# Kernel optimization log

Measured on AMD Instinct MI355X. Metric: run time of the kernel, lower is better.

The kernel has to match this reference:

```python
import jax, jax.numpy as jnp
import numpy as np

B, DIM, HEADS, AGENT = 16, 256, 8, 49
POOL = 7  # int(sqrt(agent_num))


def _pool_matrix(size, out):
    # PyTorch AdaptiveAvgPool2d bin boundaries: start=floor(i*size/out), end=ceil((i+1)*size/out)
    P = np.zeros((out, size), np.float32)
    for i in range(out):
        s = (i * size) // out
        e = -((-(i + 1) * size) // out)
        P[i, s:e] = 1.0 / (e - s)
    return jnp.asarray(P)


def _forward(x, Wq, Wkv, Wproj, bproj, Wdwc, bdwc,
             an_bias, na_bias, ah_bias, aw_bias, ha_bias, wa_bias, H, W):
    b, c, h, w = x.shape
    n = H * W
    head_dim = c // HEADS
    scale = head_dim ** -0.5
    xt = x.reshape(b, c, n).transpose(0, 2, 1)            # [b, n, c]
    q = xt @ Wq.T                                          # [b, n, c]
    kv = xt @ Wkv.T
    k, v = jnp.split(kv, 2, axis=-1)
    # agent tokens: adaptive avg pool of q over the HxW grid -> 7x7
    qimg = q.reshape(b, H, W, c)
    Ph, Pw = _pool_matrix(H, POOL), _pool_matrix(W, POOL)
    agent = jnp.einsum('ph,qw,bhwc->bpqc', Ph, Pw, qimg).reshape(b, AGENT, c)

    def to_heads(t):
        return t.reshape(b, -1, HEADS, head_dim).transpose(0, 2, 1, 3)

    qh, kh, vh, ah = to_heads(q), to_heads(k), to_heads(v), to_heads(agent)

    # stage 1: agent -> kv attention with interpolated position bias
    pb1 = jax.image.resize(an_bias, (HEADS, AGENT, H, W), method='bilinear').reshape(HEADS, AGENT, n)
    pb2 = (ah_bias + aw_bias).reshape(1, HEADS, AGENT, n)
    pos_bias = pb1[None] + pb2                             # [1/b, h, 49, n]
    agent_attn = jax.nn.softmax(jnp.einsum('bhad,bhnd->bhan', ah * scale, kh) + pos_bias, axis=-1)
    agent_v = jnp.einsum('bhan,bhnd->bhad', agent_attn, vh)  # [b, h, 49, d]

    # stage 2: query -> agent attention
    ab1 = jax.image.resize(na_bias, (HEADS, AGENT, H, W), method='bilinear').reshape(HEADS, AGENT, n).transpose(0, 2, 1)
    ab2 = (ha_bias + wa_bias).reshape(1, HEADS, n, AGENT)
    agent_bias = ab1[None] + ab2                           # [1/b, h, n, 49]
    q_attn = jax.nn.softmax(jnp.einsum('bhnd,bhad->bhna', qh * scale, ah) + agent_bias, axis=-1)
    out = jnp.einsum('bhna,bhad->bhnd', q_attn, agent_v).transpose(0, 2, 1, 3).reshape(b, n, c)

    # depthwise conv residual on v
    vimg = vh.transpose(0, 2, 1, 3).reshape(b, H, W, c).transpose(0, 3, 1, 2)  # [b, c, H, W]
    dw = jax.lax.conv_general_dilated(vimg, Wdwc, (1, 1), 'SAME',
                                      feature_group_count=c,
                                      dimension_numbers=('NCHW', 'OIHW', 'NCHW'))
    dw = dw + bdwc[None, :, None, None]
    out = out + dw.transpose(0, 2, 3, 1).reshape(b, n, c)
    out = out @ Wproj.T + bproj
    return out.transpose(0, 2, 1).reshape(b, c, h, w)


def setup_inputs() -> dict:
    key = jax.random.key(0)
    ks = jax.random.split(key, 12)
    s = 0.02
    return {
        'x': jax.random.normal(ks[0], (B, DIM, 64, 64), jnp.float32),
        'Wq': jax.random.normal(ks[1], (DIM, DIM), jnp.float32) * s,
        'Wkv': jax.random.normal(ks[2], (2 * DIM, DIM), jnp.float32) * s,
        'Wproj': jax.random.normal(ks[3], (DIM, DIM), jnp.float32) * s,
        'bproj': jnp.zeros((DIM,), jnp.float32),
        'Wdwc': jax.random.normal(ks[4], (DIM, 1, 3, 3), jnp.float32) * s,
        'bdwc': jnp.zeros((DIM,), jnp.float32),
        'an_bias': jax.random.normal(ks[5], (HEADS, AGENT, 7, 7), jnp.float32) * s,
        'na_bias': jax.random.normal(ks[6], (HEADS, AGENT, 7, 7), jnp.float32) * s,
        'ah_bias': jax.random.normal(ks[7], (1, HEADS, AGENT, 64, 1), jnp.float32) * s,
        'aw_bias': jax.random.normal(ks[8], (1, HEADS, AGENT, 1, 64), jnp.float32) * s,
        'ha_bias': jax.random.normal(ks[9], (1, HEADS, 64, 1, AGENT), jnp.float32) * s,
        'wa_bias': jax.random.normal(ks[10], (1, HEADS, 1, 64, AGENT), jnp.float32) * s,
        'H': 64,
        'W': 64,
    }


def reference(x, Wq, Wkv, Wproj, bproj, Wdwc, bdwc,
              an_bias, na_bias, ah_bias, aw_bias, ha_bias, wa_bias, H, W):
    return _forward(x, Wq, Wkv, Wproj, bproj, Wdwc, bdwc,
                    an_bias, na_bias, ah_bias, aw_bias, ha_bias, wa_bias, H, W)
```

## Files before the change

### kernel.cpp

```cpp
#include <hip/hip_runtime.h>
#include <hip/hip_bf16.h>
#include <stdint.h>

using bf16 = __hip_bfloat16;

#define SCALE 0.17677669529663687f

typedef short short8 __attribute__((ext_vector_type(8)));
typedef float f32x4 __attribute__((ext_vector_type(4)));

__device__ __forceinline__ float bf2f(bf16 v) { return __bfloat162float(v); }

__device__ __forceinline__ unsigned short f2bf(float f) {
    unsigned int u = __float_as_uint(f);
    unsigned int r = u + 0x7fffu + ((u >> 16) & 1u);
    return (unsigned short)(r >> 16);
}

__device__ __forceinline__ void load8bf(const bf16* p, float* f) {
    uint4 u = *reinterpret_cast<const uint4*>(p);
    f[0] = __uint_as_float(u.x << 16); f[1] = __uint_as_float(u.x & 0xffff0000u);
    f[2] = __uint_as_float(u.y << 16); f[3] = __uint_as_float(u.y & 0xffff0000u);
    f[4] = __uint_as_float(u.z << 16); f[5] = __uint_as_float(u.z & 0xffff0000u);
    f[6] = __uint_as_float(u.w << 16); f[7] = __uint_as_float(u.w & 0xffff0000u);
}

__device__ __forceinline__ void gload16(const void* g, void* l) {
    __builtin_amdgcn_global_load_lds(
        (const __attribute__((address_space(1))) void*)g,
        (__attribute__((address_space(3))) void*)l, 16, 0, 0);
}

__global__ __launch_bounds__(256) void convert_w(
    const float* __restrict__ Wq, const float* __restrict__ Wkv,
    const float* __restrict__ Wp,
    bf16* __restrict__ Wqkv_bf, bf16* __restrict__ Wp_bf)
{
    int row = blockIdx.x, tid = threadIdx.x;
    const float* src; bf16* dst;
    if (row < 768) {
        src = (row < 256) ? Wq + (size_t)row * 256 : Wkv + (size_t)(row - 256) * 256;
        dst = Wqkv_bf + (size_t)row * 256;
    } else {
        src = Wp + (size_t)(row - 768) * 256;
        dst = Wp_bf + (size_t)(row - 768) * 256;
    }
    *reinterpret_cast<unsigned short*>(dst + tid) = f2bf(src[tid]);
}

__global__ __launch_bounds__(256) void x_to_bf16T(
    const float* __restrict__ x, bf16* __restrict__ xT)
{
    __shared__ float t[64][65];
    const int b = blockIdx.z, pos0 = blockIdx.x * 64, c0 = blockIdx.y * 64;
    const int tid = threadIdx.x;
    const int cc = tid >> 6, p = tid & 63;
    #pragma unroll
    for (int i = 0; i < 16; ++i)
        t[cc + 4 * i][p] = x[((size_t)(b * 256 + c0 + cc + 4 * i)) * 4096 + pos0 + p];
    __syncthreads();
    const int pl = tid >> 2, qd = tid & 3;
    unsigned short tmp[16];
    #pragma unroll
    for (int j = 0; j < 16; ++j) tmp[j] = f2bf(t[qd * 16 + j][pl]);
    uint4* dst = reinterpret_cast<uint4*>(xT + ((size_t)(b * 4096 + pos0 + pl)) * 256 + c0 + qd * 16);
    dst[0] = reinterpret_cast<const uint4*>(tmp)[0];
    dst[1] = reinterpret_cast<const uint4*>(tmp)[1];
}

__global__ __launch_bounds__(256) void qkv_mfma(
    const bf16* __restrict__ xT, const bf16* __restrict__ Wqkv,
    bf16* __restrict__ q, bf16* __restrict__ k, bf16* __restrict__ v)
{
    __shared__ __align__(16) short As[128 * 32];
    __shared__ __align__(16) short Bs[128 * 32];
    const int b = blockIdx.x >> 5;
    const int m0 = (blockIdx.x & 31) * 128;
    const int j0 = blockIdx.y * 128;
    const int tid = threadIdx.x;
    const int w = tid >> 6, lane = tid & 63;
    const int wm = w & 1, wn = w >> 1;
    const int quad = lane >> 4, ln = lane & 15;

    const short* Ag = (const short*)xT + ((size_t)(b * 4096 + m0)) * 256;
    const short* Bg = (const short*)Wqkv + (size_t)j0 * 256;
    const int ldrow = lane >> 2;
    const int ldcol = (lane & 3) * 8;

    f32x4 acc[4][4] = {};

    for (int k0 = 0; k0 < 256; k0 += 32) {
        __syncthreads();
        #pragma unroll
        for (int p = 0; p < 2; ++p) {
            int row = w * 32 + p * 16;
            gload16(Ag + (size_t)(row + ldrow) * 256 + k0 + ldcol, As + row * 32);
            gload16(Bg + (size_t)(row + ldrow) * 256 + k0 + ldcol, Bs + row * 32);
        }
        __syncthreads();
        short8 af[4], bfr[4];
        #pragma unroll
        for (int mi = 0; mi < 4; ++mi)
            af[mi] = *reinterpret_cast<const short8*>(&As[(wm * 64 + mi * 16 + ln) * 32 + quad * 8]);
        #pragma unroll
        for (int ni = 0; ni < 4; ++ni)
            bfr[ni] = *reinterpret_cast<const short8*>(&Bs[(wn * 64 + ni * 16 + ln) * 32 + quad * 8]);
        #pragma unroll
        for (int mi = 0; mi < 4; ++mi)
            #pragma unroll
            for (int ni = 0; ni < 4; ++ni)
                acc[mi][ni] = __builtin_amdgcn_mfma_f32_16x16x32_bf16(
                    af[mi], bfr[ni], acc[mi][ni], 0, 0, 0);
    }

    bf16* dst; int cb;
    if (j0 < 256)      { dst = q; cb = j0; }
    else if (j0 < 512) { dst = k; cb = j0 - 256; }
    else               { dst = v; cb = j0 - 512; }
    #pragma unroll
    for (int mi = 0; mi < 4; ++mi)
        #pragma unroll
        for (int r = 0; r < 4; ++r) {
            int pos = m0 + wm * 64 + mi * 16 + quad * 4 + r;
            unsigned short* o = reinterpret_cast<unsigned short*>(
                dst + ((size_t)(b * 4096 + pos)) * 256 + cb + wn * 64 + ln);
            #pragma unroll
            for (int ni = 0; ni < 4; ++ni)
                o[ni * 16] = f2bf(acc[mi][ni][r]);
        }
}

__global__ __launch_bounds__(256) void pool_agent(
    const bf16* __restrict__ q, float* __restrict__ agent)
{
    int bid = blockIdx.x;
    int b = bid / 49, a = bid % 49;
    int py = a / 7, px = a % 7;
    int ys = (py * 64) / 7, ye = ((py + 1) * 64 + 6) / 7;
    int xs = (px * 64) / 7, xe = ((px + 1) * 64 + 6) / 7;
    int ch = threadIdx.x;
    float s = 0.f;
    for (int y = ys; y < ye; ++y)
        for (int x = xs; x < xe; ++x)
            s += bf2f(q[((size_t)(b * 4096) + y * 64 + x) * 256 + ch]);
    agent[((size_t)(b * 49) + a) * 256 + ch] = s / (float)((ye - ys) * (xe - xs));
}

__global__ __launch_bounds__(256) void make_pbias(
    const float* __restrict__ an, const float* __restrict__ ahb,
    const float* __restrict__ awb, float* __restrict__ pbias)
{
    int bid = blockIdx.x;
    __shared__ float bb[49], ay[64], ax[64];
    int tid = threadIdx.x;
    if (tid < 49) bb[tid] = an[(size_t)bid * 49 + tid];
    if (tid < 64) {
        ay[tid] = ahb[(size_t)bid * 64 + tid];
        ax[tid] = awb[(size_t)bid * 64 + tid];
    }
    __syncthreads();
    for (int it = 0; it < 16; ++it) {
        int pos = it * 256 + tid;
        int y = pos >> 6, x = pos & 63;
        float fy = (y + 0.5f) * (7.f / 64.f) - 0.5f; fy = fminf(fmaxf(fy, 0.f), 6.f);
        float fx = (x + 0.5f) * (7.f / 64.f) - 0.5f; fx = fminf(fmaxf(fx, 0.f), 6.f);
        int y0 = (int)fy, x0 = (int)fx;
        int y1 = min(y0 + 1, 6), x1 = min(x0 + 1, 6);
        float wy = fy - y0, wx = fx - x0;
        float val = (1.f - wy) * ((1.f - wx) * bb[y0 * 7 + x0] + wx * bb[y0 * 7 + x1])
                  + wy * ((1.f - wx) * bb[y1 * 7 + x0] + wx * bb[y1 * 7 + x1]);
        pbias[(size_t)bid * 4096 + pos] = val + ay[y] + ax[x];
    }
}

__global__ __launch_bounds__(256) void make_abias(
    const float* __restrict__ na, const float* __restrict__ hab,
    const float* __restrict__ wab, float* __restrict__ abiasT)
{
    int bid = blockIdx.x;
    int h = bid / 49, a = bid % 49;
    __shared__ float bb[49], hy[64], wx_[64];
    int tid = threadIdx.x;
    if (tid < 49) bb[tid] = na[(size_t)bid * 49 + tid];
    if (tid < 64) {
        hy[tid]  = hab[((size_t)(h * 64) + tid) * 49 + a];
        wx_[tid] = wab[((size_t)(h * 64) + tid) * 49 + a];
    }
    __syncthreads();
    for (int it = 0; it < 16; ++it) {
        int pos = it * 256 + tid;
        int y = pos >> 6, x = pos & 63;
        float fy = (y + 0.5f) * (7.f / 64.f) - 0.5f; fy = fminf(fmaxf(fy, 0.f), 6.f);
        float fx = (x + 0.5f) * (7.f / 64.f) - 0.5f; fx = fminf(fmaxf(fx, 0.f), 6.f);
        int y0 = (int)fy, x0 = (int)fx;
        int y1 = min(y0 + 1, 6), x1 = min(x0 + 1, 6);
        float wy = fy - y0, wxv = fx - x0;
        float val = (1.f - wy) * ((1.f - wxv) * bb[y0 * 7 + x0] + wxv * bb[y0 * 7 + x1])
                  + wy * ((1.f - wxv) * bb[y1 * 7 + x0] + wxv * bb[y1 * 7 + x1]);
        abiasT[(size_t)bid * 4096 + pos] = val + hy[y] + wx_[x];
    }
}

__global__ __launch_bounds__(256) void stage1(
    const float* __restrict__ agent, const bf16* __restrict__ k,
    const bf16* __restrict__ v, const float* __restrict__ pbias,
    float* __restrict__ part_O, float* __restrict__ part_sum)
{
    const int bid = blockIdx.x;
    const int split = bid & 7, h = (bid >> 3) & 7, b = bid >> 6;
    const int tid = threadIdx.x;
    __shared__ float e_lds[64 * 129];

    const int n_loc = tid & 127;
    const int half  = __builtin_amdgcn_readfirstlane(tid >> 7);
    const int a0 = half * 25, na = half ? 24 : 25;
    const int wv   = __builtin_amdgcn_readfirstlane(tid >> 6);
    const int lane = tid & 63;
    const int aL = lane < 49 ? lane : 48;

    float o[8] = {0.f, 0.f, 0.f, 0.f, 0.f, 0.f, 0.f, 0.f};
    float sacc = 0.f;

    for (int tile = 0; tile < 4; ++tile) {
        const int nbase = split * 512 + tile * 128;
        __syncthreads();
        {
            const int n_glob = nbase + n_loc;
            float kf[32];
            const bf16* kr = k + ((size_t)(b * 4096) + n_glob) * 256 + h * 32;
            load8bf(kr, kf); load8bf(kr + 8, kf + 8);
            load8bf(kr + 16, kf + 16); load8bf(kr + 24, kf + 24);
            const float* aqb = agent + ((size_t)(b * 49) + a0) * 256 + h * 32;
            const float* pbb = pbias + ((size_t)(h * 49) + a0) * 4096 + n_glob;
            for (int ai = 0; ai < na; ++ai) {
                const float* aq = aqb + (size_t)ai * 256;
                float dot = 0.f;
                #pragma unroll
                for (int d = 0; d < 32; ++d) dot = fmaf(aq[d], kf[d], dot);
                float s = dot * SCALE + pbb[(size_t)ai * 4096];
                e_lds[(a0 + ai) * 129 + n_loc] = __expf(s);
            }
        }
        __syncthreads();
        {
            const uint4* vrow = reinterpret_cast<const uint4*>(
                v + ((size_t)(b * 4096) + nbase) * 256 + h * 32 + wv * 8);
            for (int nn = 0; nn < 128; ++nn) {
                float e = e_lds[aL * 129 + nn];
                uint4 pk = vrow[(size_t)nn * 32];
                float vf[8];
                vf[0] = __uint_as_float(pk.x << 16); vf[1] = __uint_as_float(pk.x & 0xffff0000u);
                vf[2] = __uint_as_float(pk.y << 16); vf[3] = __uint_as_float(pk.y & 0xffff0000u);
                vf[4] = __uint_as_float(pk.z << 16); vf[5] = __uint_as_float(pk.z & 0xffff0000u);
                vf[6] = __uint_as_float(pk.w << 16); vf[7] = __uint_as_float(pk.w & 0xffff0000u);
                #pragma unroll
                for (int j = 0; j < 8; ++j) o[j] = fmaf(e, vf[j], o[j]);
                sacc += e;
            }
        }
    }
    if (lane < 49) {
        float* dst = part_O + ((size_t)((b * 8 + h) * 8 + split)) * 1568 + lane * 32 + wv * 8;
        float4 w0 = make_float4(o[0], o[1], o[2], o[3]);
        float4 w1 = make_float4(o[4], o[5], o[6], o[7]);
        *reinterpret_cast<float4*>(dst)     = w0;
        *reinterpret_cast<float4*>(dst + 4) = w1;
        if (wv == 0)
            part_sum[((b * 8 + h) * 8 + split) * 49 + lane] = sacc;
    }
}

__global__ __launch_bounds__(256) void stage1_fin(
    const float* __restrict__ part_O, const float* __restrict__ part_sum,
    float* __restrict__ agent_v)
{
    int bh = blockIdx.x;
    __shared__ float inv[49];
    int tid = threadIdx.x;
    if (tid < 49) {
        float s = 0.f;
        #pragma unroll
        for (int sp = 0; sp < 8; ++sp) s += part_sum[(bh * 8 + sp) * 49 + tid];
        inv[tid] = 1.f / s;
    }
    __syncthreads();
    for (int idx = tid; idx < 1568; idx += 256) {
        float o = 0.f;
        #pragma unroll
        for (int sp = 0; sp < 8; ++sp) o += part_O[((size_t)(bh * 8) + sp) * 1568 + idx];
        agent_v[(size_t)bh * 1568 + idx] = o * inv[idx >> 5];
    }
}

__global__ __launch_bounds__(256) void stage2(
    const bf16* __restrict__ q, const bf16* __restrict__ v,
    const float* __restrict__ agent, const float* __restrict__ agent_v,
    const float* __restrict__ abiasT, const float* __restrict__ wdwc,
    const float* __restrict__ bdwc, bf16* __restrict__ mid)
{
    const int bh = blockIdx.x;
    const int b = bh >> 3, h = bh & 7;
    const int pos = blockIdx.y * 256 + threadIdx.x;

    const float* agb = agent + ((size_t)(b * 49)) * 256 + h * 32;
    const float* avb = agent_v + (size_t)bh * 1568;
    const float* abb = abiasT + (size_t)(h * 49) * 4096 + pos;
    const float* wdb = wdwc + (size_t)(h * 32) * 9;
    const float* bdb = bdwc + h * 32;

    float qv[32];
    {
        const bf16* qr = q + ((size_t)(b * 4096) + pos) * 256 + h * 32;
        #pragma unroll
        for (int u = 0; u < 4; ++u) {
            float f[8]; load8bf(qr + u * 8, f);
            #pragma unroll
            for (int d = 0; d < 8; ++d) qv[u * 8 + d] = f[d] * SCALE;
        }
    }

    float sum = 0.f;
    float acc[32];
    #pragma unroll
    for (int d = 0; d < 32; ++d) acc[d] = 0.f;

    for (int a = 0; a < 49; ++a) {
        const float* ag = agb + (size_t)a * 256;
        const float* av = avb + a * 32;
        float t = abb[(size_t)a * 4096];
        #pragma unroll
        for (int d = 0; d < 32; ++d) t = fmaf(qv[d], ag[d], t);
        float e = __expf(t);
        sum += e;
        #pragma unroll
        for (int d = 0; d < 32; ++d) acc[d] = fmaf(e, av[d], acc[d]);
    }
    float inv = 1.f / sum;
    #pragma unroll
    for (int d = 0; d < 32; ++d) acc[d] *= inv;

    int y = pos >> 6, x = pos & 63;
    #pragma unroll
    for (int dy = -1; dy <= 1; ++dy) {
        int yy = y + dy; if (yy < 0 || yy > 63) continue;
        #pragma unroll
        for (int dx = -1; dx <= 1; ++dx) {
            int xx = x + dx; if (xx < 0 || xx > 63) continue;
            const bf16* vr = v + ((size_t)(b * 4096) + yy * 64 + xx) * 256 + h * 32;
            int widx = (dy + 1) * 3 + (dx + 1);
            #pragma unroll
            for (int u = 0; u < 4; ++u) {
                float f[8]; load8bf(vr + u * 8, f);
                #pragma unroll
                for (int d = 0; d < 8; ++d)
                    acc[u * 8 + d] = fmaf(wdb[(u * 8 + d) * 9 + widx], f[d], acc[u * 8 + d]);
            }
        }
    }
    #pragma unroll
    for (int d = 0; d < 32; ++d) acc[d] += bdb[d];

    bf16* dst = mid + ((size_t)(b * 4096) + pos) * 256 + h * 32;
    #pragma unroll
    for (int u = 0; u < 4; ++u) {
        ushort4 w;
        w.x = f2bf(acc[u * 8 + 0]);
        w.y = f2bf(acc[u * 8 + 1]);
        w.z = f2bf(acc[u * 8 + 2]);
        w.w = f2bf(acc[u * 8 + 3]);
        ushort4 w2;
        w2.x = f2bf(acc[u * 8 + 4]);
        w2.y = f2bf(acc[u * 8 + 5]);
        w2.z = f2bf(acc[u * 8 + 6]);
        w2.w = f2bf(acc[u * 8 + 7]);
        *reinterpret_cast<ushort4*>(dst + u * 8)     = w;
        *reinterpret_cast<ushort4*>(dst + u * 8 + 4) = w2;
    }
}

__global__ __launch_bounds__(256) void proj_mfma(
    const bf16* __restrict__ mid, const bf16* __restrict__ Wp,
    const float* __restrict__ bp, float* __restrict__ out)
{
    __shared__ __align__(16) short As[128 * 32];
    __shared__ __align__(16) short Bs[128 * 32];
    const int m0 = blockIdx.x * 128;
    const int b  = blockIdx.y >> 5;
    const int n0 = (blockIdx.y & 31) * 128;
    const int tid = threadIdx.x;
    const int w = tid >> 6, lane = tid & 63;
    const int wm = w & 1, wn = w >> 1;
    const int quad = lane >> 4, ln = lane & 15;

    const short* Ag = (const short*)Wp + (size_t)m0 * 256;
    const short* Bg = (const short*)mid + ((size_t)(b * 4096 + n0)) * 256;
    const int ldrow = lane >> 2;
    const int ldcol = (lane & 3) * 8;

    f32x4 acc[4][4] = {};

    for (int k0 = 0; k0 < 256; k0 += 32) {
        __syncthreads();
        #pragma unroll
        for (int p = 0; p < 2; ++p) {
            int row = w * 32 + p * 16;
            gload16(Ag + (size_t)(row + ldrow) * 256 + k0 + ldcol, As + row * 32);
            gload16(Bg + (size_t)(row + ldrow) * 256 + k0 + ldcol, Bs + row * 32);
        }
        __syncthreads();
        short8 af[4], bfr[4];
        #pragma unroll
        for (int mi = 0; mi < 4; ++mi)
            af[mi] = *reinterpret_cast<const short8*>(&As[(wm * 64 + mi * 16 + ln) * 32 + quad * 8]);
        #pragma unroll
        for (int ni = 0; ni < 4; ++ni)
            bfr[ni] = *reinterpret_cast<const short8*>(&Bs[(wn * 64 + ni * 16 + ln) * 32 + quad * 8]);
        #pragma unroll
        for (int mi = 0; mi < 4; ++mi)
            #pragma unroll
            for (int ni = 0; ni < 4; ++ni)
                acc[mi][ni] = __builtin_amdgcn_mfma_f32_16x16x32_bf16(
                    af[mi], bfr[ni], acc[mi][ni], 0, 0, 0);
    }

    #pragma unroll
    for (int mi = 0; mi < 4; ++mi)
        #pragma unroll
        for (int r = 0; r < 4; ++r) {
            int ch = m0 + wm * 64 + mi * 16 + quad * 4 + r;
            float bias = bp[ch];
            float* o = out + ((size_t)(b * 256 + ch)) * 4096 + n0 + wn * 64 + ln;
            #pragma unroll
            for (int ni = 0; ni < 4; ++ni)
                o[ni * 16] = acc[mi][ni][r] + bias;
        }
}

extern "C" void kernel_launch(void* const* d_in, const int* in_sizes, int n_in,
                              void* d_out, int out_size, void* d_ws, size_t ws_size,
                              hipStream_t stream)
{
    const float* x       = (const float*)d_in[0];
    const float* Wq      = (const float*)d_in[1];
    const float* Wkv     = (const float*)d_in[2];
    const float* Wproj   = (const float*)d_in[3];
    const float* bproj   = (const float*)d_in[4];
    const float* Wdwc    = (const float*)d_in[5];
    const float* bdwc    = (const float*)d_in[6];
    const float* an_bias = (const float*)d_in[7];
    const float* na_bias = (const float*)d_in[8];
    const float* ah_bias = (const float*)d_in[9];
    const float* aw_bias = (const float*)d_in[10];
    const float* ha_bias = (const float*)d_in[11];
    const float* wa_bias = (const float*)d_in[12];

    char* ws = (char*)d_ws;
    bf16*  q      = (bf16*)(ws + 0);
    bf16*  k      = (bf16*)(ws + 33554432);
    bf16*  v      = (bf16*)(ws + 67108864);
    bf16*  xT     = (bf16*)(ws + 100663296);
    float* part_O   = (float*)(ws + 100663296);
    float* part_sum = (float*)(ws + 100663296 + 6422528);
    bf16*  mid    = (bf16*)(ws + 100663296);
    float* agent  = (float*)(ws + 134217728);
    float* agentv = (float*)(ws + 135020544);
    float* pbias  = (float*)(ws + 135823360);
    float* abiasT = (float*)(ws + 142245888);
    bf16*  Wqkv_bf = (bf16*)(ws + 148668416);
    bf16*  Wp_bf   = (bf16*)(ws + 149061632);
    float* out    = (float*)d_out;

    convert_w <<<dim3(1024),     256, 0, stream>>>(Wq, Wkv, Wproj, Wqkv_bf, Wp_bf);
    x_to_bf16T<<<dim3(64, 4, 16),256, 0, stream>>>(x, xT);
    qkv_mfma  <<<dim3(512, 6),   256, 0, stream>>>(xT, Wqkv_bf, q, k, v);
    pool_agent<<<dim3(784),      256, 0, stream>>>(q, agent);
    make_pbias<<<dim3(392),      256, 0, stream>>>(an_bias, ah_bias, aw_bias, pbias);
    make_abias<<<dim3(392),      256, 0, stream>>>(na_bias, ha_bias, wa_bias, abiasT);
    stage1    <<<dim3(1024),     256, 0, stream>>>(agent, k, v, pbias, part_O, part_sum);
    stage1_fin<<<dim3(128),      256, 0, stream>>>(part_O, part_sum, agentv);
    stage2    <<<dim3(128, 16),  256, 0, stream>>>(q, v, agent, agentv, abiasT, Wdwc, bdwc, mid);
    proj_mfma <<<dim3(2, 512),   256, 0, stream>>>(mid, Wp_bf, bproj, out);
}
```

Baseline: 442.6 us.

## Rewrite stage1 agent attention with bf16 MFMA for scores and PV

Stage1 now computes the agent-key scores and the probability-times-V products with 16x16x32 bf16 MFMA instructions instead of scalar FMA loops. Agent queries are staged in LDS as bf16, V is transposed into LDS, and the exponentiated scores are rounded to bf16 in LDS for the second MFMA. The aim is to cut the FP32 ALU work and LDS traffic of this stage. In exchange the probabilities and agent queries lose precision through the bf16 rounding, and 15 of the 64 padded agent rows are computed and then discarded.

```diff
diff --git a/kernel.cpp b/kernel.cpp
--- a/kernel.cpp
+++ b/kernel.cpp
@@ -209,64 +209,96 @@
     const int bid = blockIdx.x;
     const int split = bid & 7, h = (bid >> 3) & 7, b = bid >> 6;
     const int tid = threadIdx.x;
-    __shared__ float e_lds[64 * 129];
-
-    const int n_loc = tid & 127;
-    const int half  = __builtin_amdgcn_readfirstlane(tid >> 7);
-    const int a0 = half * 25, na = half ? 24 : 25;
-    const int wv   = __builtin_amdgcn_readfirstlane(tid >> 6);
-    const int lane = tid & 63;
-    const int aL = lane < 49 ? lane : 48;
-
-    float o[8] = {0.f, 0.f, 0.f, 0.f, 0.f, 0.f, 0.f, 0.f};
-    float sacc = 0.f;
-
-    for (int tile = 0; tile < 4; ++tile) {
-        const int nbase = split * 512 + tile * 128;
+    const int w = tid >> 6, lane = tid & 63;
+    const int ln = lane & 15, quad = lane >> 4;
+
+    __shared__ __align__(16) short agLds[64 * 32];
+    __shared__ __align__(16) short pLds[64 * 140];
+    __shared__ __align__(16) short vtLds[32 * 140];
+
+    for (int i = tid; i < 64 * 32; i += 256) {
+        int a = i >> 5, d = i & 31;
+        float val = (a < 49) ? agent[((size_t)(b * 49) + a) * 256 + h * 32 + d] : 0.f;
+        agLds[i] = (short)f2bf(val);
+    }
+    __syncthreads();
+
+    const short8 agFrag = *reinterpret_cast<const short8*>(&agLds[(w * 16 + ln) * 32 + quad * 8]);
+    const int a_row = w * 16 + quad * 4;
+
+    f32x4 oAcc[2] = {};
+    float sacc[4] = {0.f, 0.f, 0.f, 0.f};
+    const f32x4 zero4 = {0.f, 0.f, 0.f, 0.f};
+
+    for (int sub = 0; sub < 4; ++sub) {
+        const int nbase = split * 512 + sub * 128;
         __syncthreads();
         {
-            const int n_glob = nbase + n_loc;
-            float kf[32];
-            const bf16* kr = k + ((size_t)(b * 4096) + n_glob) * 256 + h * 32;
-            load8bf(kr, kf); load8bf(kr + 8, kf + 8);
-            load8bf(kr + 16, kf + 16); load8bf(kr + 24, kf + 24);
-            const float* aqb = agent + ((size_t)(b * 49) + a0) * 256 + h * 32;
-            const float* pbb = pbias + ((size_t)(h * 49) + a0) * 4096 + n_glob;
-            for (int ai = 0; ai < na; ++ai) {
-                const float* aq = aqb + (size_t)ai * 256;
-                float dot = 0.f;
-                #pragma unroll
-                for (int d = 0; d < 32; ++d) dot = fmaf(aq[d], kf[d], dot);
-                float s = dot * SCALE + pbb[(size_t)ai * 4096];
-                e_lds[(a0 + ai) * 129 + n_loc] = __expf(s);
+            const int n_loc = tid & 127, dh = (tid >> 7) * 16;
+            const short* vr = (const short*)v + ((size_t)(b * 4096) + nbase + n_loc) * 256 + h * 32 + dh;
+            uint4 u0 = *reinterpret_cast<const uint4*>(vr);
+            uint4 u1 = *reinterpret_cast<const uint4*>(vr + 8);
+            unsigned int uu[8] = {u0.x, u0.y, u0.z, u0.w, u1.x, u1.y, u1.z, u1.w};
+            #pragma unroll
+            for (int j = 0; j < 8; ++j) {
+                vtLds[(dh + 2 * j) * 140 + n_loc]     = (short)(uu[j] & 0xffffu);
+                vtLds[(dh + 2 * j + 1) * 140 + n_loc] = (short)(uu[j] >> 16);
             }
         }
+        short8 kf[8];
+        #pragma unroll
+        for (int t = 0; t < 8; ++t) {
+            int n = nbase + t * 16 + ln;
+            kf[t] = *reinterpret_cast<const short8*>(
+                (const short*)k + ((size_t)(b * 4096) + n) * 256 + h * 32 + quad * 8);
+        }
+        #pragma unroll
+        for (int t = 0; t < 8; ++t) {
+            f32x4 s = __builtin_amdgcn_mfma_f32_16x16x32_bf16(agFrag, kf[t], zero4, 0, 0, 0);
+            int n = nbase + t * 16 + ln;
+            #pragma unroll
+            for (int r = 0; r < 4; ++r) {
+                int a = a_row + r;
+                float e = 0.f;
+                if (a < 49) {
+                    float sv = s[r] * SCALE + pbias[((size_t)(h * 49) + a) * 4096 + n];
+                    e = __expf(sv);
+                }
+                sacc[r] += e;
+                pLds[(a_row + r) * 140 + t * 16 + ln] = (short)f2bf(e);
+            }
+        }
         __syncthreads();
-        {
-            const uint4* vrow = reinterpret_cast<const uint4*>(
-                v + ((size_t)(b * 4096) + nbase) * 256 + h * 32 + wv * 8);
-            for (int nn = 0; nn < 128; ++nn) {
-                float e = e_lds[aL * 129 + nn];
-                uint4 pk = vrow[(size_t)nn * 32];
-                float vf[8];
-                vf[0] = __uint_as_float(pk.x << 16); vf[1] = __uint_as_float(pk.x & 0xffff0000u);
-                vf[2] = __uint_as_float(pk.y << 16); vf[3] = __uint_as_float(pk.y & 0xffff0000u);
-                vf[4] = __uint_as_float(pk.z << 16); vf[5] = __uint_as_float(pk.z & 0xffff0000u);
-                vf[6] = __uint_as_float(pk.w << 16); vf[7] = __uint_as_float(pk.w & 0xffff0000u);
-                #pragma unroll
-                for (int j = 0; j < 8; ++j) o[j] = fmaf(e, vf[j], o[j]);
-                sacc += e;
+        #pragma unroll
+        for (int ks = 0; ks < 4; ++ks) {
+            short8 pf = *reinterpret_cast<const short8*>(&pLds[(w * 16 + ln) * 140 + ks * 32 + quad * 8]);
+            #pragma unroll
+            for (int dt = 0; dt < 2; ++dt) {
+                short8 vf = *reinterpret_cast<const short8*>(&vtLds[(dt * 16 + ln) * 140 + ks * 32 + quad * 8]);
+                oAcc[dt] = __builtin_amdgcn_mfma_f32_16x16x32_bf16(pf, vf, oAcc[dt], 0, 0, 0);
             }
         }
     }
-    if (lane < 49) {
-        float* dst = part_O + ((size_t)((b * 8 + h) * 8 + split)) * 1568 + lane * 32 + wv * 8;
-        float4 w0 = make_float4(o[0], o[1], o[2], o[3]);
-        float4 w1 = make_float4(o[4], o[5], o[6], o[7]);
-        *reinterpret_cast<float4*>(dst)     = w0;
-        *reinterpret_cast<float4*>(dst + 4) = w1;
-        if (wv == 0)
-            part_sum[((b * 8 + h) * 8 + split) * 49 + lane] = sacc;
+
+    const size_t obase = ((size_t)((b * 8 + h) * 8 + split)) * 1568;
+    #pragma unroll
+    for (int dt = 0; dt < 2; ++dt)
+        #pragma unroll
+        for (int r = 0; r < 4; ++r) {
+            int a = a_row + r;
+            if (a < 49)
+                part_O[obase + a * 32 + dt * 16 + ln] = oAcc[dt][r];
+        }
+    #pragma unroll
+    for (int r = 0; r < 4; ++r) {
+        float sv = sacc[r];
+        #pragma unroll
+        for (int m = 1; m < 16; m <<= 1) sv += __shfl_xor(sv, m, 64);
+        if (ln == 0) {
+            int a = a_row + r;
+            if (a < 49)
+                part_sum[((b * 8 + h) * 8 + split) * 49 + a] = sv;
+        }
     }
 }
 
```

Result: faster. 391.3 us (-11.6%).
